# Performance work log

Measured on AMD Instinct MI355X. Metric: run time of the kernel, lower is better.

The kernel has to match this reference:

```python
import jax, jax.numpy as jnp
import numpy as np

B, N, G, P, L = 2, 6, 4, 8, 4
CIN, COUT = 256, 128
CIMG = COUT // G  # 32 per-group image channels
CAMC = 64
GX, GY, GZ = 64, 64, 4
Q = 8192
RES = (0.6, 0.6, 0.4)
PR = (-19.2, -19.2, -1.0)
IMG_W, IMG_H = 704.0, 256.0
FEAT_HW = [(32, 88), (16, 44), (8, 22), (4, 11)]


def setup_inputs():
    key = jax.random.key(0)
    ks = jax.random.split(key, 20)
    inp = {}
    for l, (H, W) in enumerate(FEAT_HW):
        inp[f"feat{l}"] = jax.random.normal(ks[l], (B, N, G * CIMG, H, W), jnp.float32)
    inp["pts_bev"] = jax.random.normal(ks[4], (B, CIN, GY, GX), jnp.float32)
    inp["lidar2img"] = jax.random.normal(ks[5], (B, N, 4, 4), jnp.float32)
    inp["query_mask"] = jnp.ones((B, Q), jnp.float32)
    inp["vox_x"] = jax.random.randint(ks[6], (B, Q), 0, GX, jnp.int32)
    inp["vox_y"] = jax.random.randint(ks[7], (B, Q), 0, GY, jnp.int32)
    inp["vox_z"] = jax.random.randint(ks[8], (B, Q), 0, GZ, jnp.int32)
    inp["w_offset"] = 0.02 * jax.random.normal(ks[9], (CIN, G * P * 3), jnp.float32)
    inp["b_offset"] = jax.random.uniform(ks[10], (G * P * 3,), jnp.float32, -0.5, 0.5)
    inp["w_scale"] = 0.02 * jax.random.normal(ks[11], (CIN, G * P * L), jnp.float32)
    inp["b_scale"] = jnp.zeros((G * P * L,), jnp.float32)
    inp["w_agg"] = 0.02 * jax.random.normal(ks[12], (P * COUT, COUT), jnp.float32)
    inp["b_agg"] = jnp.zeros((COUT,), jnp.float32)
    inp["conv1_w"] = 0.02 * jax.random.normal(ks[13], (CAMC * GZ, COUT * GZ, 3, 3), jnp.float32)
    inp["conv2_w"] = 0.02 * jax.random.normal(ks[14], (512, CAMC * GZ, 3, 3), jnp.float32)
    inp["conv3_w"] = 0.02 * jax.random.normal(ks[15], (512, 512, 3, 3), jnp.float32)
    inp["conv4_w"] = 0.02 * jax.random.normal(ks[16], (COUT, 512, 3, 3), jnp.float32)
    for i, c in zip(range(1, 5), (CAMC * GZ, 512, 512, COUT)):
        inp[f"bn{i}_g"] = jnp.ones((c,), jnp.float32)
        inp[f"bn{i}_b"] = jnp.zeros((c,), jnp.float32)
    return inp


def _bilinear(feat, bg, view, u, v):
    # feat: [BG, N, H, W, C]; u, v normalized to [0,1]; zero padding, align_corners=False
    H, W = feat.shape[2], feat.shape[3]
    px = u * W - 0.5
    py = v * H - 0.5
    x0f = jnp.floor(px)
    y0f = jnp.floor(py)
    wx = px - x0f
    wy = py - y0f
    x0 = x0f.astype(jnp.int32)
    y0 = y0f.astype(jnp.int32)

    def g(xi, yi):
        ok = ((xi >= 0) & (xi < W) & (yi >= 0) & (yi < H)).astype(feat.dtype)
        val = feat[bg, view, jnp.clip(yi, 0, H - 1), jnp.clip(xi, 0, W - 1)]
        return val * ok[..., None]

    return (g(x0, y0) * ((1 - wx) * (1 - wy))[..., None]
            + g(x0 + 1, y0) * (wx * (1 - wy))[..., None]
            + g(x0, y0 + 1) * ((1 - wx) * wy)[..., None]
            + g(x0 + 1, y0 + 1) * (wx * wy)[..., None])


def _conv_bn_relu(x, w, g, b):
    y = jax.lax.conv_general_dilated(x, w, (1, 1), 'SAME',
                                     dimension_numbers=('NCHW', 'OIHW', 'NCHW'))
    # eval-mode BatchNorm with running_mean=0, running_var=1
    y = y * (g / np.float32(np.sqrt(1.0 + 1e-5)))[None, :, None, None] + b[None, :, None, None]
    return jax.nn.relu(y)


def reference(feat0, feat1, feat2, feat3, pts_bev, lidar2img, query_mask,
              w_offset, b_offset, w_scale, b_scale, w_agg, b_agg,
              conv1_w, bn1_g, bn1_b, conv2_w, bn2_g, bn2_b,
              conv3_w, bn3_g, bn3_b, conv4_w, bn4_g, bn4_b,
              vox_x, vox_y, vox_z):
    GP = G * P
    bidx = jnp.arange(B)[:, None]
    # sparse voxel gather of BEV point features (pts_feat[i, y, x])
    pts_f = pts_bev.transpose(0, 2, 3, 1)[bidx, vox_y, vox_x]  # [B,Q,CIN]
    off = (pts_f @ w_offset + b_offset).reshape(B, Q, GP, 3)
    sw = jax.nn.softmax((pts_f @ w_scale + b_scale).reshape(B, Q, GP, L), axis=-1)
    # frustum voxel-center coords
    coord = jnp.stack([(vox_x + 0.5) * RES[0] + PR[0],
                       (vox_y + 0.5) * RES[1] + PR[1],
                       (vox_z + 0.5) * RES[2] + PR[2]], axis=-1).astype(jnp.float32)
    # make_sample_points: xy scaled by res[0], z by res[2]
    delta = off * jnp.array([RES[0], RES[0], RES[2]], jnp.float32)
    sxyz = coord[:, :, None, :] + delta  # [B,Q,GP,3]
    sp4 = jnp.concatenate([sxyz, jnp.ones_like(sxyz[..., :1])], axis=-1)
    cam = jnp.einsum('bnij,bqpj->bnqpi', lidar2img, sp4)  # [B,N,Q,GP,4]
    homo = jnp.maximum(cam[..., 2:3], 1e-5)
    uv = cam[..., 0:2] / homo / jnp.array([IMG_W, IMG_H], jnp.float32)
    valid = ((cam[..., 2] > 1e-5) & (uv[..., 0] > 0.0) & (uv[..., 0] < 1.0)
             & (uv[..., 1] > 0.0) & (uv[..., 1] < 1.0)).astype(jnp.float32)
    valid = valid.transpose(0, 2, 3, 1)  # [B,Q,GP,N]
    i_view = jnp.argmax(valid, axis=-1)  # [B,Q,GP]
    uv_q = uv.transpose(0, 2, 3, 1, 4)  # [B,Q,GP,N,2]
    idx = jnp.broadcast_to(i_view[..., None, None], (B, Q, GP, 1, 2))
    uv_sel = jnp.take_along_axis(uv_q, idx, axis=3)[..., 0, :]  # [B,Q,GP,2]
    # split heads/groups -> [B*G, Q, P, *]
    uv_bg = uv_sel.reshape(B, Q, G, P, 2).transpose(0, 2, 1, 3, 4).reshape(B * G, Q, P, 2)
    view_bg = i_view.reshape(B, Q, G, P).transpose(0, 2, 1, 3).reshape(B * G, Q, P)
    sw_bg = sw.reshape(B, Q, G, P, L).transpose(0, 2, 1, 3, 4).reshape(B * G, Q, P, L)
    bg = jnp.arange(B * G)[:, None, None]
    # msmv_sampling: multi-level multi-view bilinear sampling + softmax level weights
    out = jnp.zeros((B * G, Q, P, CIMG), jnp.float32)
    for l, f in enumerate((feat0, feat1, feat2, feat3)):
        H, W = f.shape[3], f.shape[4]
        fv = f.reshape(B, N, G, CIMG, H, W).transpose(0, 2, 1, 4, 5, 3).reshape(B * G, N, H, W, CIMG)
        out = out + sw_bg[..., l:l + 1] * _bilinear(fv, bg, view_bg, uv_bg[..., 0], uv_bg[..., 1])
    # [B,G,Q,P,C] -> [B,Q,P,G,C] -> flatten (matches final.permute(0,2,4,1,3).flatten(2))
    final = out.reshape(B, G, Q, P, CIMG).transpose(0, 2, 3, 1, 4).reshape(B, Q, P * G * CIMG)
    agg = final @ w_agg + b_agg  # [B,Q,COUT]
    # scatter back into dense BEV grid
    ffeat = jnp.zeros((B, GZ, GY, GX, COUT), jnp.float32)
    ffeat = ffeat.at[bidx, vox_z, vox_y, vox_x].add(agg * query_mask[..., None])
    x = ffeat.transpose(0, 4, 1, 2, 3).reshape(B, COUT * GZ, GY, GX)
    x = _conv_bn_relu(x, conv1_w, bn1_g, bn1_b)
    x = _conv_bn_relu(x, conv2_w, bn2_g, bn2_b)
    x = _conv_bn_relu(x, conv3_w, bn3_g, bn3_b)
    return _conv_bn_relu(x, conv4_w, bn4_g, bn4_b)
```

## Files before the change

kernel.cpp:

```cpp
#include <hip/hip_runtime.h>
#include <hip/hip_fp16.h>
#include <math.h>

#define NB    2
#define NQ    8192
#define NCIN  256
#define NG    4
#define NP    8
#define NGP   32
#define NCIMG 32
#define NCOUT 128
#define NVIEW 6
#define GXD   64
#define GYD   64
#define GZD   4

typedef float f32x4 __attribute__((ext_vector_type(4)));
typedef short s16x8 __attribute__((ext_vector_type(8)));
typedef unsigned short u16;
typedef unsigned int   u32;

__device__ __forceinline__ u16 bf16_rne(float f) {
    u32 u = __float_as_uint(f);
    u32 r = (u + 0x7FFFu + ((u >> 16) & 1u)) >> 16;
    return (u16)r;
}
__device__ __forceinline__ float bf16_f(u16 h) {
    return __uint_as_float(((u32)h) << 16);
}

__global__ void transpose_feat(const float* __restrict__ src, float* __restrict__ dst,
                               int H, int W)
{
    const int total = NB * NG * NVIEW * H * W * 32;
    for (int i = blockIdx.x * blockDim.x + threadIdx.x; i < total;
         i += gridDim.x * blockDim.x) {
        int c = i & 31;
        int r = i >> 5;
        int x = r % W;  r /= W;
        int y = r % H;  r /= H;
        int n = r % NVIEW; r /= NVIEW;
        int g = r & 3;  r >>= 2;
        int b = r;
        dst[i] = src[(((size_t)(b * NVIEW + n) * 128 + g * 32 + c) * H + y) * W + x];
    }
}

__global__ __launch_bounds__(256) void transpose_pts(const float* __restrict__ src,
                                                     float* __restrict__ dst)
{
    __shared__ float tile[64][65];
    const int tid = blockIdx.x;
    const int b = tid >> 8, rest = tid & 255;
    const int p0 = (rest >> 2) << 6, c0 = (rest & 3) << 6;
    const int t = threadIdx.x;
    for (int i = t; i < 4096; i += 256) {
        const int c = i >> 6, p = i & 63;
        tile[c][p] = src[((size_t)(b * 256 + c0 + c) << 12) + p0 + p];
    }
    __syncthreads();
    for (int i = t; i < 4096; i += 256) {
        const int p = i >> 6, c = i & 63;
        dst[((size_t)(b * 4096) + p0 + p) * 256 + c0 + c] = tile[c][p];
    }
}

__global__ void pack_wT(const float* __restrict__ w_off, const float* __restrict__ w_sc,
                        float* __restrict__ wT)
{
    int i = blockIdx.x * 256 + threadIdx.x;
    if (i >= 224 * 256) return;
    int col = i >> 8, k = i & 255;
    wT[i] = (col < 96) ? w_off[k * 96 + col] : w_sc[k * 128 + (col - 96)];
}

__global__ void pack_wagT(const float* __restrict__ w_agg, u16* __restrict__ dst)
{
    int i = blockIdx.x * 256 + threadIdx.x;
    if (i >= 128 * 1024) return;
    int co = i >> 10, k = i & 1023;
    dst[i] = bf16_rne(w_agg[k * 128 + co]);
}

__global__ void pack_conv_w(const float* __restrict__ src, u16* __restrict__ hi,
                            u16* __restrict__ lo, int CI, int CO)
{
    const int N = CO * CI * 9;
    for (int i = blockIdx.x * blockDim.x + threadIdx.x; i < N;
         i += gridDim.x * blockDim.x) {
        int tap = i % 9;
        int r = i / 9;
        int ci = r % CI;
        int co = r / CI;
        float v = src[i];
        u16 h = bf16_rne(v);
        size_t d = ((size_t)tap * CO + co) * CI + ci;
        hi[d] = h;
        lo[d] = bf16_rne(v - bf16_f(h));
    }
}

__global__ void split_x0(const float* __restrict__ x, u16* __restrict__ h,
                         u16* __restrict__ lo)
{
    const int N = NB * 4096 * 512;
    for (int i = blockIdx.x * blockDim.x + threadIdx.x; i < N;
         i += gridDim.x * blockDim.x) {
        float v = x[i];
        u16 hh = bf16_rne(v);
        h[i] = hh;
        lo[i] = bf16_rne(v - bf16_f(hh));
    }
}

__global__ __launch_bounds__(256) void fused_query8(
    const float* __restrict__ pts_cl, const float* __restrict__ l2i,
    const float* __restrict__ qmask,
    const float* __restrict__ wT, const float* __restrict__ b_off,
    const float* __restrict__ b_sc,
    const u16* __restrict__ wagT, const float* __restrict__ b_agg,
    const int* __restrict__ vxp, const int* __restrict__ vyp, const int* __restrict__ vzp,
    const float* __restrict__ fT,
    float* __restrict__ xout_cl)
{
    const int q0 = blockIdx.x << 3;
    const int b  = q0 >> 13;
    const int t  = threadIdx.x;

    __shared__ float s_pts[8][256];
    __shared__ float s_off[8][96];
    __shared__ float s_sw[8][128];
    __shared__ float s_l2i[96];
    __shared__ u32   s_toff[256][16];
    __shared__ u16   s_twgt[256][16];
    __shared__ __align__(16) u16 s_fh[8][1024];
    __shared__ __align__(16) u16 s_fl[8][1024];
    __shared__ int   s_vx[8], s_vy[8], s_vz[8];
    __shared__ float s_qm[8];

    if (t < 8) {
        s_vx[t] = vxp[q0 + t]; s_vy[t] = vyp[q0 + t]; s_vz[t] = vzp[q0 + t];
        s_qm[t] = qmask[q0 + t];
    }
    if (t < 96) s_l2i[t] = l2i[b * 96 + t];
    __syncthreads();

    #pragma unroll
    for (int q = 0; q < 8; ++q)
        s_pts[q][t] = pts_cl[((size_t)(b * 4096) + s_vy[q] * 64 + s_vx[q]) * 256 + t];
    __syncthreads();

    if (t < 224) {
        const float* __restrict__ wrow = wT + t * 256;
        const float bias = (t < 96) ? b_off[t] : b_sc[t - 96];
        float a0 = bias, a1 = bias, a2 = bias, a3 = bias;
        float a4 = bias, a5 = bias, a6 = bias, a7 = bias;
        #pragma unroll 4
        for (int k = 0; k < 256; ++k) {
            const float wk = wrow[k];
            a0 = fmaf(s_pts[0][k], wk, a0); a1 = fmaf(s_pts[1][k], wk, a1);
            a2 = fmaf(s_pts[2][k], wk, a2); a3 = fmaf(s_pts[3][k], wk, a3);
            a4 = fmaf(s_pts[4][k], wk, a4); a5 = fmaf(s_pts[5][k], wk, a5);
            a6 = fmaf(s_pts[6][k], wk, a6); a7 = fmaf(s_pts[7][k], wk, a7);
        }
        if (t < 96) {
            s_off[0][t] = a0; s_off[1][t] = a1; s_off[2][t] = a2; s_off[3][t] = a3;
            s_off[4][t] = a4; s_off[5][t] = a5; s_off[6][t] = a6; s_off[7][t] = a7;
        } else {
            const int c = t - 96;
            s_sw[0][c] = a0; s_sw[1][c] = a1; s_sw[2][c] = a2; s_sw[3][c] = a3;
            s_sw[4][c] = a4; s_sw[5][c] = a5; s_sw[6][c] = a6; s_sw[7][c] = a7;
        }
    }
    __syncthreads();

    {
        const int q = t >> 5, gp = t & 31;
        float a0 = s_sw[q][gp * 4 + 0], a1 = s_sw[q][gp * 4 + 1];
        float a2 = s_sw[q][gp * 4 + 2], a3 = s_sw[q][gp * 4 + 3];
        float m  = fmaxf(fmaxf(a0, a1), fmaxf(a2, a3));
        float e0 = expf(a0 - m), e1 = expf(a1 - m), e2 = expf(a2 - m), e3 = expf(a3 - m);
        float inv = 1.f / (e0 + e1 + e2 + e3);
        const float sw0 = e0 * inv, sw1 = e1 * inv, sw2 = e2 * inv, sw3 = e3 * inv;

        float cx = ((float)s_vx[q] + 0.5f) * 0.6f - 19.2f;
        float cy = ((float)s_vy[q] + 0.5f) * 0.6f - 19.2f;
        float cz = ((float)s_vz[q] + 0.5f) * 0.4f - 1.0f;
        float sx = cx + s_off[q][gp * 3 + 0] * 0.6f;
        float sy = cy + s_off[q][gp * 3 + 1] * 0.6f;
        float sz = cz + s_off[q][gp * 3 + 2] * 0.4f;

        int best = 0; float bu = 0.f, bv = 0.f; bool found = false;
        #pragma unroll
        for (int n = 0; n < NVIEW; ++n) {
            const float* M = &s_l2i[n * 16];
            float px = M[0] * sx + M[1] * sy + M[2]  * sz + M[3];
            float py = M[4] * sx + M[5] * sy + M[6]  * sz + M[7];
            float pz = M[8] * sx + M[9] * sy + M[10] * sz + M[11];
            float homo = fmaxf(pz, 1e-5f);
            float u = px / homo / 704.0f;
            float v = py / homo / 256.0f;
            bool val = (pz > 1e-5f) && (u > 0.f) && (u < 1.f) && (v > 0.f) && (v < 1.f);
            if (n == 0) { bu = u; bv = v; }
            if (val && !found) { found = true; best = n; bu = u; bv = v; }
        }

        const int g = gp >> 3;
        const u32 bgv = (u32)((b * 4 + g) * 6 + best);
        auto tapgen = [&](int lidx, int W, int H, u32 lbase, float swl) {
            float px = fminf(fmaxf(bu * (float)W - 0.5f, -1.0e8f), 1.0e8f);
            float py = fminf(fmaxf(bv * (float)H - 0.5f, -1.0e8f), 1.0e8f);
            float x0f = floorf(px), y0f = floorf(py);
            float wx = px - x0f, wy = py - y0f;
            int x0 = (int)x0f, y0 = (int)y0f;
            const u32 base = lbase + bgv * (u32)(H * W * 32);
            #pragma unroll
            for (int ti = 0; ti < 4; ++ti) {
                int xi = x0 + (ti & 1), yi = y0 + (ti >> 1);
                float bw = ((ti & 1) ? wx : 1.f - wx) * ((ti >> 1) ? wy : 1.f - wy);
                bool ok = ((unsigned)xi < (unsigned)W) && ((unsigned)yi < (unsigned)H);
                u32 off = ok ? (base + ((u32)(yi * W + xi) << 5)) : 0u;
                float wgt = ok ? swl * bw : 0.f;
                s_toff[t][lidx * 4 + ti] = off;
                s_twgt[t][lidx * 4 + ti] = __half_as_ushort(__float2half(wgt));
            }
        };
        tapgen(0, 88, 32, 0u,       sw0);
        tapgen(1, 44, 16, 4325376u, sw1);
        tapgen(2, 22,  8, 5406720u, sw2);
        tapgen(3, 11,  4, 5677056u, sw3);
    }
    __syncthreads();

    for (int i = t; i < 8192; i += 256) {
        const int pair = i >> 5, c = i & 31;
        float acc = 0.f;
        #pragma unroll
        for (int tp = 0; tp < 16; ++tp) {
            const u32 off = s_toff[pair][tp];
            const float wgt = __half2float(__ushort_as_half(s_twgt[pair][tp]));
            acc = fmaf(wgt, fT[off + c], acc);
        }
        const int gp = pair & 31, q = pair >> 5;
        const int g = gp >> 3, p = gp & 7;
        const int k = ((p << 2) + g) * 32 + c;
        const u16 h  = bf16_rne(acc);
        const u16 lo = bf16_rne(acc - bf16_f(h));
        const int kk = (((k >> 3) ^ q) << 3) | (k & 7);
        s_fh[q][kk] = h;
        s_fl[q][kk] = lo;
    }
    __syncthreads();

    {
        const int wv = t >> 6, l = t & 63;
        const int l15 = l & 15, kg = l >> 4;
        f32x4 acc0 = {0.f, 0.f, 0.f, 0.f}, acc1 = {0.f, 0.f, 0.f, 0.f};
        const u16* __restrict__ B0 = wagT + (((wv * 2) * 16 + l15) << 10);
        const u16* __restrict__ B1 = wagT + (((wv * 2 + 1) * 16 + l15) << 10);
        const bool realA = (l15 < 8);
        for (int ks = 0; ks < 32; ++ks) {
            s16x8 Ah = {0, 0, 0, 0, 0, 0, 0, 0};
            s16x8 Al = {0, 0, 0, 0, 0, 0, 0, 0};
            if (realA) {
                const int kk = ((((ks << 2) + kg) ^ l15) << 3);
                Ah = *reinterpret_cast<const s16x8*>(&s_fh[l15][kk]);
                Al = *reinterpret_cast<const s16x8*>(&s_fl[l15][kk]);
            }
            const int ko = (ks << 5) + (kg << 3);
            const s16x8 Bh0 = *reinterpret_cast<const s16x8*>(B0 + ko);
            const s16x8 Bh1 = *reinterpret_cast<const s16x8*>(B1 + ko);
            acc0 = __builtin_amdgcn_mfma_f32_16x16x32_bf16(Ah, Bh0, acc0, 0, 0, 0);
            acc0 = __builtin_amdgcn_mfma_f32_16x16x32_bf16(Al, Bh0, acc0, 0, 0, 0);
            acc1 = __builtin_amdgcn_mfma_f32_16x16x32_bf16(Ah, Bh1, acc1, 0, 0, 0);
            acc1 = __builtin_amdgcn_mfma_f32_16x16x32_bf16(Al, Bh1, acc1, 0, 0, 0);
        }
        if (l < 32) {
            #pragma unroll
            for (int reg = 0; reg < 4; ++reg) {
                const int q = kg * 4 + reg;
                const size_t pbase =
                    ((size_t)(b * 4096) + s_vy[q] * 64 + s_vx[q]) * 512 + s_vz[q];
                const float qm = s_qm[q];
                {
                    const int co = (wv * 2) * 16 + l15;
                    atomicAdd(&xout_cl[pbase + co * 4], (acc0[reg] + b_agg[co]) * qm);
                }
                {
                    const int co = (wv * 2 + 1) * 16 + l15;
                    atomicAdd(&xout_cl[pbase + co * 4], (acc1[reg] + b_agg[co]) * qm);
                }
            }
        }
    }
}

template<int ROWS, int NSUB, bool LAST>
__global__ __launch_bounds__(64 * ROWS * NSUB) void conv3x3_mfma2(
    const u16* __restrict__ xinh, const u16* __restrict__ xinl,
    const u16* __restrict__ whi, const u16* __restrict__ wlo,
    const float* __restrict__ gam, const float* __restrict__ bet,
    u16* __restrict__ youth, u16* __restrict__ youtl,
    float* __restrict__ ynchw, int CI, int CO)
{
    constexpr int STRIPS = 64 / ROWS;
    constexpr int NTHR = 64 * ROWS * NSUB;
    constexpr int SR = ROWS + 2;
    const int b = blockIdx.x / STRIPS, s = blockIdx.x % STRIPS;
    const int y0 = s * ROWS;
    const int co0 = blockIdx.y * (NSUB * 32);
    const int t = threadIdx.x;
    const int wid = t >> 6, l = t & 63;
    const int l15 = l & 15, kg = l >> 4;
    const int r = wid / NSUB, ns = wid % NSUB;

    __shared__ __align__(16) u16 sh[SR * 66 * 32];
    __shared__ __align__(16) u16 sl[SR * 66 * 32];

    const int coA = co0 + ns * 32 + l15;
    const int coB = coA + 16;

    f32x4 acc[4][2];
    #pragma unroll
    for (int m = 0; m < 4; ++m) {
        acc[m][0] = (f32x4){0.f, 0.f, 0.f, 0.f};
        acc[m][1] = (f32x4){0.f, 0.f, 0.f, 0.f};
    }

    for (int cc = 0; cc < CI; cc += 32) {
        __syncthreads();
        for (int i = t; i < SR * 66 * 4; i += NTHR) {
            const int cb = i & 3, r2 = i >> 2;
            const int xx = r2 % 66, rr = r2 / 66;
            const int yi = y0 - 1 + rr, xi = xx - 1;
            uint4 H = {0, 0, 0, 0}, L = {0, 0, 0, 0};
            if ((unsigned)yi < 64u && (unsigned)xi < 64u) {
                const size_t src = ((size_t)(b * 4096 + yi * 64 + xi)) * CI + cc + cb * 8;
                H = *reinterpret_cast<const uint4*>(xinh + src);
                L = *reinterpret_cast<const uint4*>(xinl + src);
            }
            const int off = (rr * 66 + xx) * 32 + ((cb ^ ((xx ^ (xx >> 2)) & 3)) << 3);
            *reinterpret_cast<uint4*>(&sh[off]) = H;
            *reinterpret_cast<uint4*>(&sl[off]) = L;
        }
        __syncthreads();

        #pragma unroll
        for (int tap = 0; tap < 9; ++tap) {
            const int ky = tap / 3, kx = tap % 3;
            const size_t woA = ((size_t)tap * CO + coA) * CI + cc + kg * 8;
            const size_t woB = ((size_t)tap * CO + coB) * CI + cc + kg * 8;
            const s16x8 BhA = *reinterpret_cast<const s16x8*>(whi + woA);
            const s16x8 BlA = *reinterpret_cast<const s16x8*>(wlo + woA);
            const s16x8 BhB = *reinterpret_cast<const s16x8*>(whi + woB);
            const s16x8 BlB = *reinterpret_cast<const s16x8*>(wlo + woB);
            #pragma unroll
            for (int m = 0; m < 4; ++m) {
                const int xx = m * 16 + l15 + kx;
                const int off = ((r + ky) * 66 + xx) * 32
                              + ((kg ^ ((xx ^ (xx >> 2)) & 3)) << 3);
                const s16x8 Ah = *reinterpret_cast<const s16x8*>(&sh[off]);
                const s16x8 Al = *reinterpret_cast<const s16x8*>(&sl[off]);
                acc[m][0] = __builtin_amdgcn_mfma_f32_16x16x32_bf16(Ah, BhA, acc[m][0], 0, 0, 0);
                acc[m][0] = __builtin_amdgcn_mfma_f32_16x16x32_bf16(Ah, BlA, acc[m][0], 0, 0, 0);
                acc[m][0] = __builtin_amdgcn_mfma_f32_16x16x32_bf16(Al, BhA, acc[m][0], 0, 0, 0);
                acc[m][1] = __builtin_amdgcn_mfma_f32_16x16x32_bf16(Ah, BhB, acc[m][1], 0, 0, 0);
                acc[m][1] = __builtin_amdgcn_mfma_f32_16x16x32_bf16(Ah, BlB, acc[m][1], 0, 0, 0);
                acc[m][1] = __builtin_amdgcn_mfma_f32_16x16x32_bf16(Al, BhB, acc[m][1], 0, 0, 0);
            }
        }
    }

    const float inv = 0.99999500003749978f;
    const int row = y0 + r;
    #pragma unroll
    for (int j = 0; j < 2; ++j) {
        const int co = j ? coB : coA;
        const float gsc = gam[co] * inv;
        const float bta = bet[co];
        #pragma unroll
        for (int m = 0; m < 4; ++m) {
            #pragma unroll
            for (int reg = 0; reg < 4; ++reg) {
                const int x = m * 16 + kg * 4 + reg;
                const float val = fmaxf(fmaf(acc[m][j][reg], gsc, bta), 0.f);
                if (LAST) {
                    ynchw[(((size_t)(b * CO + co)) << 12) + row * 64 + x] = val;
                } else {
                    const size_t idx = ((size_t)(b * 4096 + row * 64 + x)) * CO + co;
                    const u16 h = bf16_rne(val);
                    youth[idx] = h;
                    youtl[idx] = bf16_rne(val - bf16_f(h));
                }
            }
        }
    }
}

extern "C" void kernel_launch(void* const* d_in, const int* in_sizes, int n_in,
                              void* d_out, int out_size, void* d_ws, size_t ws_size,
                              hipStream_t stream)
{
    const float* feat0    = (const float*)d_in[0];
    const float* feat1    = (const float*)d_in[1];
    const float* feat2    = (const float*)d_in[2];
    const float* feat3    = (const float*)d_in[3];
    const float* pts_bev  = (const float*)d_in[4];
    const float* l2i      = (const float*)d_in[5];
    const float* qmask    = (const float*)d_in[6];
    const int*   vox_x    = (const int*)d_in[7];
    const int*   vox_y    = (const int*)d_in[8];
    const int*   vox_z    = (const int*)d_in[9];
    const float* w_off    = (const float*)d_in[10];
    const float* b_off    = (const float*)d_in[11];
    const float* w_sc     = (const float*)d_in[12];
    const float* b_sc     = (const float*)d_in[13];
    const float* w_agg    = (const float*)d_in[14];
    const float* b_agg    = (const float*)d_in[15];
    const float* conv1_w  = (const float*)d_in[16];
    const float* conv2_w  = (const float*)d_in[17];
    const float* conv3_w  = (const float*)d_in[18];
    const float* conv4_w  = (const float*)d_in[19];
    const float* bn1_g    = (const float*)d_in[20];
    const float* bn1_b    = (const float*)d_in[21];
    const float* bn2_g    = (const float*)d_in[22];
    const float* bn2_b    = (const float*)d_in[23];
    const float* bn3_g    = (const float*)d_in[24];
    const float* bn3_b    = (const float*)d_in[25];
    const float* bn4_g    = (const float*)d_in[26];
    const float* bn4_b    = (const float*)d_in[27];

    char* wsb = (char*)d_ws;
    float* fT0 = (float*)wsb;
    float* fT1 = fT0 + 4325376;
    float* fT2 = fT1 + 1081344;
    float* fT3 = fT2 + 270336;
    u16* wpk = (u16*)wsb;
    u16* wh1 = wpk;             u16* wl1 = wpk + 1179648;
    u16* wh2 = wpk + 2359296;   u16* wl2 = wpk + 3538944;
    u16* wh3 = wpk + 4718592;   u16* wl3 = wpk + 7077888;
    u16* wh4 = wpk + 9437184;   u16* wl4 = wpk + 10027008;
    float* x0f   = (float*)(wsb + 22978560);
    u16*   x2h   = (u16*)(wsb + 22978560);   u16* x2l = x2h + 4194304;
    float* ptsCL = (float*)(wsb + 39755776);
    u16*   x0h   = (u16*)(wsb + 39755776);
    u16*   x0l   = (u16*)(wsb + 48144384);
    u16*   x3h   = x0h;                      u16* x3l = x0l;
    u16*   x1h   = (u16*)(wsb + 56532992);   u16* x1l = x1h + 2097152;
    u16*   wagT  = (u16*)(wsb + 48144384);
    float* wTp   = (float*)(wsb + 48406528);

    pack_wT<<<224, 256, 0, stream>>>(w_off, w_sc, wTp);
    pack_wagT<<<512, 256, 0, stream>>>(w_agg, wagT);
    transpose_pts<<<512, 256, 0, stream>>>(pts_bev, ptsCL);

    transpose_feat<<<1024, 256, 0, stream>>>(feat0, fT0, 32, 88);
    transpose_feat<<< 512, 256, 0, stream>>>(feat1, fT1, 16, 44);
    transpose_feat<<< 128, 256, 0, stream>>>(feat2, fT2,  8, 22);
    transpose_feat<<<  64, 256, 0, stream>>>(feat3, fT3,  4, 11);

    hipMemsetAsync(x0f, 0, (size_t)4194304 * sizeof(float), stream);

    fused_query8<<<NB * NQ / 8, 256, 0, stream>>>(
        ptsCL, l2i, qmask, wTp, b_off, b_sc, wagT, b_agg,
        vox_x, vox_y, vox_z, fT0, x0f);

    pack_conv_w<<<1024, 256, 0, stream>>>(conv1_w, wh1, wl1, 512, 256);
    pack_conv_w<<<1024, 256, 0, stream>>>(conv2_w, wh2, wl2, 256, 512);
    pack_conv_w<<<2048, 256, 0, stream>>>(conv3_w, wh3, wl3, 512, 512);
    pack_conv_w<<< 512, 256, 0, stream>>>(conv4_w, wh4, wl4, 512, 128);

    split_x0<<<4096, 256, 0, stream>>>(x0f, x0h, x0l);

    conv3x3_mfma2<2, 2, false><<<dim3(64, 4), 256, 0, stream>>>(
        x0h, x0l, wh1, wl1, bn1_g, bn1_b, x1h, x1l, nullptr, 512, 256);
    conv3x3_mfma2<2, 2, false><<<dim3(64, 8), 256, 0, stream>>>(
        x1h, x1l, wh2, wl2, bn2_g, bn2_b, x2h, x2l, nullptr, 256, 512);
    conv3x3_mfma2<2, 2, false><<<dim3(64, 8), 256, 0, stream>>>(
        x2h, x2l, wh3, wl3, bn3_g, bn3_b, x3h, x3l, nullptr, 512, 512);
    conv3x3_mfma2<1, 2, true><<<dim3(128, 2), 128, 0, stream>>>(
        x3h, x3l, wh4, wl4, bn4_g, bn4_b, nullptr, nullptr, (float*)d_out, 512, 128);
}
```

Measured before the change: 891.5 us.

## Switch conv chain to single fp16 MFMA and use MFMA for offset projection

The four 3x3 convs move from split-bf16 (three MFMAs per product, hi/lo activations and weights) to single-pass fp16 MFMA, with a new double-buffered LDS tile of one output row and 64 output channels per block. The offset/scale projection in the query kernel becomes a split-bf16 MFMA GEMM instead of scalar FMAs. The sampling loop now uses float4 channel loads, and LDS buffers are unioned to cut shared memory use. This removes much of the MFMA and memory traffic in the convs, but fp16 precision and range may loosen accuracy against the fp32 reference.

After: 1.170 ms. 31.2% more time.

```diff
diff --git a/kernel.cpp b/kernel.cpp
--- a/kernel.cpp
+++ b/kernel.cpp
@@ -17,6 +17,7 @@
 
 typedef float f32x4 __attribute__((ext_vector_type(4)));
 typedef short s16x8 __attribute__((ext_vector_type(8)));
+typedef _Float16 f16x8 __attribute__((ext_vector_type(8)));
 typedef unsigned short u16;
 typedef unsigned int   u32;
 
@@ -27,6 +28,9 @@
 }
 __device__ __forceinline__ float bf16_f(u16 h) {
     return __uint_as_float(((u32)h) << 16);
+}
+__device__ __forceinline__ u16 f16_u(float f) {
+    return __half_as_ushort(__float2half(f));
 }
 
 __global__ void transpose_feat(const float* __restrict__ src, float* __restrict__ dst,
@@ -65,13 +69,18 @@
     }
 }
 
-__global__ void pack_wT(const float* __restrict__ w_off, const float* __restrict__ w_sc,
-                        float* __restrict__ wT)
+__global__ void pack_wT_split(const float* __restrict__ w_off,
+                              const float* __restrict__ w_sc,
+                              u16* __restrict__ wTh, u16* __restrict__ wTl)
 {
     int i = blockIdx.x * 256 + threadIdx.x;
-    if (i >= 224 * 256) return;
+    if (i >= 256 * 256) return;
     int col = i >> 8, k = i & 255;
-    wT[i] = (col < 96) ? w_off[k * 96 + col] : w_sc[k * 128 + (col - 96)];
+    float v = (col < 96) ? w_off[k * 96 + col]
+            : (col < 224 ? w_sc[k * 128 + (col - 96)] : 0.f);
+    u16 h = bf16_rne(v);
+    wTh[col * 256 + k] = h;
+    wTl[col * 256 + k] = bf16_rne(v - bf16_f(h));
 }
 
 __global__ void pack_wagT(const float* __restrict__ w_agg, u16* __restrict__ dst)
@@ -82,8 +91,8 @@
     dst[i] = bf16_rne(w_agg[k * 128 + co]);
 }
 
-__global__ void pack_conv_w(const float* __restrict__ src, u16* __restrict__ hi,
-                            u16* __restrict__ lo, int CI, int CO)
+__global__ void pack_conv_w_f16(const float* __restrict__ src, u16* __restrict__ dst,
+                                int CI, int CO)
 {
     const int N = CO * CI * 9;
     for (int i = blockIdx.x * blockDim.x + threadIdx.x; i < N;
@@ -92,32 +101,27 @@
         int r = i / 9;
         int ci = r % CI;
         int co = r / CI;
-        float v = src[i];
-        u16 h = bf16_rne(v);
-        size_t d = ((size_t)tap * CO + co) * CI + ci;
-        hi[d] = h;
-        lo[d] = bf16_rne(v - bf16_f(h));
-    }
-}
-
-__global__ void split_x0(const float* __restrict__ x, u16* __restrict__ h,
-                         u16* __restrict__ lo)
-{
-    const int N = NB * 4096 * 512;
-    for (int i = blockIdx.x * blockDim.x + threadIdx.x; i < N;
+        dst[((size_t)tap * CO + co) * CI + ci] = f16_u(src[i]);
+    }
+}
+
+__global__ void cvt_x0(const float* __restrict__ x, u16* __restrict__ y)
+{
+    const int N4 = NB * 4096 * 512 / 4;
+    for (int i = blockIdx.x * blockDim.x + threadIdx.x; i < N4;
          i += gridDim.x * blockDim.x) {
-        float v = x[i];
-        u16 hh = bf16_rne(v);
-        h[i] = hh;
-        lo[i] = bf16_rne(v - bf16_f(hh));
+        float4 v = reinterpret_cast<const float4*>(x)[i];
+        u32 lo = (u32)f16_u(v.x) | ((u32)f16_u(v.y) << 16);
+        u32 hi = (u32)f16_u(v.z) | ((u32)f16_u(v.w) << 16);
+        reinterpret_cast<uint2*>(y)[i] = make_uint2(lo, hi);
     }
 }
 
 __global__ __launch_bounds__(256) void fused_query8(
     const float* __restrict__ pts_cl, const float* __restrict__ l2i,
     const float* __restrict__ qmask,
-    const float* __restrict__ wT, const float* __restrict__ b_off,
-    const float* __restrict__ b_sc,
+    const u16* __restrict__ wTh, const u16* __restrict__ wTl,
+    const float* __restrict__ b_off, const float* __restrict__ b_sc,
     const u16* __restrict__ wagT, const float* __restrict__ b_agg,
     const int* __restrict__ vxp, const int* __restrict__ vyp, const int* __restrict__ vzp,
     const float* __restrict__ fT,
@@ -127,16 +131,19 @@
     const int b  = q0 >> 13;
     const int t  = threadIdx.x;
 
-    __shared__ float s_pts[8][256];
+    __shared__ __align__(16) u16 s_ph[8][256];
+    __shared__ __align__(16) u16 s_pl[8][256];
     __shared__ float s_off[8][96];
     __shared__ float s_sw[8][128];
     __shared__ float s_l2i[96];
-    __shared__ u32   s_toff[256][16];
-    __shared__ u16   s_twgt[256][16];
-    __shared__ __align__(16) u16 s_fh[8][1024];
-    __shared__ __align__(16) u16 s_fl[8][1024];
+    __shared__ __align__(16) char s_un[32768];
     __shared__ int   s_vx[8], s_vy[8], s_vz[8];
     __shared__ float s_qm[8];
+
+    u32  (*s_toff)[16]  = reinterpret_cast<u32 (*)[16]>(s_un);
+    u16  (*s_twgt)[16]  = reinterpret_cast<u16 (*)[16]>(s_un + 16384);
+    u16  (*s_fh)[1024]  = reinterpret_cast<u16 (*)[1024]>(s_un);
+    u16  (*s_fl)[1024]  = reinterpret_cast<u16 (*)[1024]>(s_un + 16384);
 
     if (t < 8) {
         s_vx[t] = vxp[q0 + t]; s_vy[t] = vyp[q0 + t]; s_vz[t] = vzp[q0 + t];
@@ -145,31 +152,59 @@
     if (t < 96) s_l2i[t] = l2i[b * 96 + t];
     __syncthreads();
 
-    #pragma unroll
-    for (int q = 0; q < 8; ++q)
-        s_pts[q][t] = pts_cl[((size_t)(b * 4096) + s_vy[q] * 64 + s_vx[q]) * 256 + t];
-    __syncthreads();
-
-    if (t < 224) {
-        const float* __restrict__ wrow = wT + t * 256;
-        const float bias = (t < 96) ? b_off[t] : b_sc[t - 96];
-        float a0 = bias, a1 = bias, a2 = bias, a3 = bias;
-        float a4 = bias, a5 = bias, a6 = bias, a7 = bias;
-        #pragma unroll 4
-        for (int k = 0; k < 256; ++k) {
-            const float wk = wrow[k];
-            a0 = fmaf(s_pts[0][k], wk, a0); a1 = fmaf(s_pts[1][k], wk, a1);
-            a2 = fmaf(s_pts[2][k], wk, a2); a3 = fmaf(s_pts[3][k], wk, a3);
-            a4 = fmaf(s_pts[4][k], wk, a4); a5 = fmaf(s_pts[5][k], wk, a5);
-            a6 = fmaf(s_pts[6][k], wk, a6); a7 = fmaf(s_pts[7][k], wk, a7);
-        }
-        if (t < 96) {
-            s_off[0][t] = a0; s_off[1][t] = a1; s_off[2][t] = a2; s_off[3][t] = a3;
-            s_off[4][t] = a4; s_off[5][t] = a5; s_off[6][t] = a6; s_off[7][t] = a7;
-        } else {
-            const int c = t - 96;
-            s_sw[0][c] = a0; s_sw[1][c] = a1; s_sw[2][c] = a2; s_sw[3][c] = a3;
-            s_sw[4][c] = a4; s_sw[5][c] = a5; s_sw[6][c] = a6; s_sw[7][c] = a7;
+    {
+        const int q = t >> 5, c8 = t & 31;
+        const float4* p = reinterpret_cast<const float4*>(
+            pts_cl + ((size_t)(b * 4096) + s_vy[q] * 64 + s_vx[q]) * 256 + c8 * 8);
+        float4 v0 = p[0], v1 = p[1];
+        float v[8] = {v0.x, v0.y, v0.z, v0.w, v1.x, v1.y, v1.z, v1.w};
+        union { u16 u[8]; uint4 q4; } H, L;
+        #pragma unroll
+        for (int j = 0; j < 8; ++j) {
+            u16 h = bf16_rne(v[j]);
+            H.u[j] = h;
+            L.u[j] = bf16_rne(v[j] - bf16_f(h));
+        }
+        const int kb = c8 ^ q;
+        *reinterpret_cast<uint4*>(&s_ph[q][kb * 8]) = H.q4;
+        *reinterpret_cast<uint4*>(&s_pl[q][kb * 8]) = L.q4;
+    }
+    __syncthreads();
+
+    {
+        const int wv = t >> 6, l = t & 63;
+        const int l15 = l & 15, kg = l >> 4;
+        const int qa = l15 & 7;
+        f32x4 acc[4];
+        #pragma unroll
+        for (int nf = 0; nf < 4; ++nf) acc[nf] = (f32x4){0.f, 0.f, 0.f, 0.f};
+        #pragma unroll
+        for (int ks = 0; ks < 8; ++ks) {
+            const int kb = (ks * 4 + kg) ^ qa;
+            const s16x8 Ah = *reinterpret_cast<const s16x8*>(&s_ph[qa][kb * 8]);
+            const s16x8 Al = *reinterpret_cast<const s16x8*>(&s_pl[qa][kb * 8]);
+            #pragma unroll
+            for (int nf = 0; nf < 4; ++nf) {
+                const int col = wv * 64 + nf * 16 + l15;
+                const size_t wo = (size_t)col * 256 + ks * 32 + kg * 8;
+                const s16x8 Bh = *reinterpret_cast<const s16x8*>(wTh + wo);
+                const s16x8 Bl = *reinterpret_cast<const s16x8*>(wTl + wo);
+                acc[nf] = __builtin_amdgcn_mfma_f32_16x16x32_bf16(Ah, Bh, acc[nf], 0, 0, 0);
+                acc[nf] = __builtin_amdgcn_mfma_f32_16x16x32_bf16(Ah, Bl, acc[nf], 0, 0, 0);
+                acc[nf] = __builtin_amdgcn_mfma_f32_16x16x32_bf16(Al, Bh, acc[nf], 0, 0, 0);
+            }
+        }
+        if (kg < 2) {
+            #pragma unroll
+            for (int nf = 0; nf < 4; ++nf) {
+                const int col = wv * 64 + nf * 16 + l15;
+                #pragma unroll
+                for (int reg = 0; reg < 4; ++reg) {
+                    const int q = kg * 4 + reg;
+                    if (col < 96)        s_off[q][col]      = acc[nf][reg] + b_off[col];
+                    else if (col < 224)  s_sw[q][col - 96]  = acc[nf][reg] + b_sc[col - 96];
+                }
+            }
         }
     }
     __syncthreads();
@@ -222,7 +257,7 @@
                 u32 off = ok ? (base + ((u32)(yi * W + xi) << 5)) : 0u;
                 float wgt = ok ? swl * bw : 0.f;
                 s_toff[t][lidx * 4 + ti] = off;
-                s_twgt[t][lidx * 4 + ti] = __half_as_ushort(__float2half(wgt));
+                s_twgt[t][lidx * 4 + ti] = f16_u(wgt);
             }
         };
         tapgen(0, 88, 32, 0u,       sw0);
@@ -232,41 +267,55 @@
     }
     __syncthreads();
 
-    for (int i = t; i < 8192; i += 256) {
-        const int pair = i >> 5, c = i & 31;
-        float acc = 0.f;
+    f32x4 sacc[8];
+    #pragma unroll
+    for (int j = 0; j < 8; ++j) {
+        const int pair = (j * 256 + t) >> 3, c4 = t & 7;
+        const u32* toff = s_toff[pair];
+        const u16* twgt = s_twgt[pair];
+        f32x4 a = (f32x4){0.f, 0.f, 0.f, 0.f};
         #pragma unroll
         for (int tp = 0; tp < 16; ++tp) {
-            const u32 off = s_toff[pair][tp];
-            const float wgt = __half2float(__ushort_as_half(s_twgt[pair][tp]));
-            acc = fmaf(wgt, fT[off + c], acc);
-        }
-        const int gp = pair & 31, q = pair >> 5;
+            const float w = __half2float(__ushort_as_half(twgt[tp]));
+            const float4 f = *reinterpret_cast<const float4*>(fT + toff[tp] + c4 * 4);
+            a[0] = fmaf(w, f.x, a[0]); a[1] = fmaf(w, f.y, a[1]);
+            a[2] = fmaf(w, f.z, a[2]); a[3] = fmaf(w, f.w, a[3]);
+        }
+        sacc[j] = a;
+    }
+    __syncthreads();
+
+    #pragma unroll
+    for (int j = 0; j < 8; ++j) {
+        const int pair = (j * 256 + t) >> 3, c4 = t & 7;
+        const int q = pair >> 5, gp = pair & 31;
         const int g = gp >> 3, p = gp & 7;
-        const int k = ((p << 2) + g) * 32 + c;
-        const u16 h  = bf16_rne(acc);
-        const u16 lo = bf16_rne(acc - bf16_f(h));
-        const int kk = (((k >> 3) ^ q) << 3) | (k & 7);
-        s_fh[q][kk] = h;
-        s_fl[q][kk] = lo;
+        const int kb = ((p << 2) + g) * 4 + (c4 >> 1);
+        const int off = ((kb ^ q) << 3) + (c4 & 1) * 4;
+        u16 h[4], lo[4];
+        #pragma unroll
+        for (int e = 0; e < 4; ++e) {
+            h[e]  = bf16_rne(sacc[j][e]);
+            lo[e] = bf16_rne(sacc[j][e] - bf16_f(h[e]));
+        }
+        *reinterpret_cast<uint2*>(&s_fh[q][off]) =
+            make_uint2((u32)h[0] | ((u32)h[1] << 16), (u32)h[2] | ((u32)h[3] << 16));
+        *reinterpret_cast<uint2*>(&s_fl[q][off]) =
+            make_uint2((u32)lo[0] | ((u32)lo[1] << 16), (u32)lo[2] | ((u32)lo[3] << 16));
     }
     __syncthreads();
 
     {
         const int wv = t >> 6, l = t & 63;
         const int l15 = l & 15, kg = l >> 4;
+        const int qa = l15 & 7;
         f32x4 acc0 = {0.f, 0.f, 0.f, 0.f}, acc1 = {0.f, 0.f, 0.f, 0.f};
         const u16* __restrict__ B0 = wagT + (((wv * 2) * 16 + l15) << 10);
         const u16* __restrict__ B1 = wagT + (((wv * 2 + 1) * 16 + l15) << 10);
-        const bool realA = (l15 < 8);
         for (int ks = 0; ks < 32; ++ks) {
-            s16x8 Ah = {0, 0, 0, 0, 0, 0, 0, 0};
-            s16x8 Al = {0, 0, 0, 0, 0, 0, 0, 0};
-            if (realA) {
-                const int kk = ((((ks << 2) + kg) ^ l15) << 3);
-                Ah = *reinterpret_cast<const s16x8*>(&s_fh[l15][kk]);
-                Al = *reinterpret_cast<const s16x8*>(&s_fl[l15][kk]);
-            }
+            const int kk = ((((ks << 2) + kg) ^ qa) << 3);
+            const s16x8 Ah = *reinterpret_cast<const s16x8*>(&s_fh[qa][kk]);
+            const s16x8 Al = *reinterpret_cast<const s16x8*>(&s_fl[qa][kk]);
             const int ko = (ks << 5) + (kg << 3);
             const s16x8 Bh0 = *reinterpret_cast<const s16x8*>(B0 + ko);
             const s16x8 Bh1 = *reinterpret_cast<const s16x8*>(B1 + ko);
@@ -295,103 +344,100 @@
     }
 }
 
-template<int ROWS, int NSUB, bool LAST>
-__global__ __launch_bounds__(64 * ROWS * NSUB) void conv3x3_mfma2(
-    const u16* __restrict__ xinh, const u16* __restrict__ xinl,
-    const u16* __restrict__ whi, const u16* __restrict__ wlo,
+template<bool LAST>
+__global__ __launch_bounds__(256) void conv3x3_f16(
+    const u16* __restrict__ xin,
+    const u16* __restrict__ wf,
     const float* __restrict__ gam, const float* __restrict__ bet,
-    u16* __restrict__ youth, u16* __restrict__ youtl,
-    float* __restrict__ ynchw, int CI, int CO)
-{
-    constexpr int STRIPS = 64 / ROWS;
-    constexpr int NTHR = 64 * ROWS * NSUB;
-    constexpr int SR = ROWS + 2;
-    const int b = blockIdx.x / STRIPS, s = blockIdx.x % STRIPS;
-    const int y0 = s * ROWS;
-    const int co0 = blockIdx.y * (NSUB * 32);
+    u16* __restrict__ yf16, float* __restrict__ ynchw, int CI, int CO)
+{
+    const int b  = blockIdx.x >> 6;
+    const int y0 = blockIdx.x & 63;
+    const int co0 = blockIdx.y << 6;
     const int t = threadIdx.x;
-    const int wid = t >> 6, l = t & 63;
+    const int wv = t >> 6, l = t & 63;
     const int l15 = l & 15, kg = l >> 4;
-    const int r = wid / NSUB, ns = wid % NSUB;
-
-    __shared__ __align__(16) u16 sh[SR * 66 * 32];
-    __shared__ __align__(16) u16 sl[SR * 66 * 32];
-
-    const int coA = co0 + ns * 32 + l15;
-    const int coB = coA + 16;
-
-    f32x4 acc[4][2];
-    #pragma unroll
-    for (int m = 0; m < 4; ++m) {
-        acc[m][0] = (f32x4){0.f, 0.f, 0.f, 0.f};
-        acc[m][1] = (f32x4){0.f, 0.f, 0.f, 0.f};
-    }
-
+
+    __shared__ __align__(16) u16 lds[2][3 * 66 * 32];
+
+    const int cnt = (t < 24) ? 4 : 3;
+    size_t soff[4]; int loff[4]; bool sval[4];
+    #pragma unroll
+    for (int k = 0; k < 4; ++k) {
+        const int i = t + k * 256;
+        const int cb = i & 3, xr = i >> 2;
+        const int x = xr % 66, r = xr / 66;
+        const int yi = y0 - 1 + r, xi = x - 1;
+        sval[k] = ((unsigned)yi < 64u) && ((unsigned)xi < 64u) && (i < 792);
+        soff[k] = ((size_t)(b * 4096 + yi * 64 + xi)) * CI + cb * 8;
+        loff[k] = (r * 66 + x) * 32 + cb * 8;
+    }
+
+    f32x4 acc[4];
+    #pragma unroll
+    for (int nf = 0; nf < 4; ++nf) acc[nf] = (f32x4){0.f, 0.f, 0.f, 0.f};
+
+    const uint4 Z = make_uint4(0u, 0u, 0u, 0u);
+    uint4 st[4];
+    #pragma unroll
+    for (int k = 0; k < 4; ++k)
+        if (k < cnt) st[k] = sval[k] ? *reinterpret_cast<const uint4*>(xin + soff[k]) : Z;
+    #pragma unroll
+    for (int k = 0; k < 4; ++k)
+        if (k < cnt && (t + k * 256) < 792)
+            *reinterpret_cast<uint4*>(&lds[0][loff[k]]) = st[k];
+    __syncthreads();
+
+    int cur = 0;
     for (int cc = 0; cc < CI; cc += 32) {
+        const bool more = (cc + 32 < CI);
+        if (more) {
+            #pragma unroll
+            for (int k = 0; k < 4; ++k)
+                if (k < cnt)
+                    st[k] = sval[k]
+                          ? *reinterpret_cast<const uint4*>(xin + soff[k] + cc + 32) : Z;
+        }
+        #pragma unroll
+        for (int ky = 0; ky < 3; ++ky) {
+            #pragma unroll
+            for (int kx = 0; kx < 3; ++kx) {
+                const f16x8 A = *reinterpret_cast<const f16x8*>(
+                    &lds[cur][(ky * 66 + wv * 16 + l15 + kx) * 32 + kg * 8]);
+                const int tap = ky * 3 + kx;
+                #pragma unroll
+                for (int nf = 0; nf < 4; ++nf) {
+                    const int co = co0 + nf * 16 + l15;
+                    const f16x8 B = *reinterpret_cast<const f16x8*>(
+                        wf + ((size_t)tap * CO + co) * CI + cc + kg * 8);
+                    acc[nf] = __builtin_amdgcn_mfma_f32_16x16x32_f16(A, B, acc[nf], 0, 0, 0);
+                }
+            }
+        }
+        if (more) {
+            #pragma unroll
+            for (int k = 0; k < 4; ++k)
+                if (k < cnt && (t + k * 256) < 792)
+                    *reinterpret_cast<uint4*>(&lds[cur ^ 1][loff[k]]) = st[k];
+        }
         __syncthreads();
-        for (int i = t; i < SR * 66 * 4; i += NTHR) {
-            const int cb = i & 3, r2 = i >> 2;
-            const int xx = r2 % 66, rr = r2 / 66;
-            const int yi = y0 - 1 + rr, xi = xx - 1;
-            uint4 H = {0, 0, 0, 0}, L = {0, 0, 0, 0};
-            if ((unsigned)yi < 64u && (unsigned)xi < 64u) {
-                const size_t src = ((size_t)(b * 4096 + yi * 64 + xi)) * CI + cc + cb * 8;
-                H = *reinterpret_cast<const uint4*>(xinh + src);
-                L = *reinterpret_cast<const uint4*>(xinl + src);
-            }
-            const int off = (rr * 66 + xx) * 32 + ((cb ^ ((xx ^ (xx >> 2)) & 3)) << 3);
-            *reinterpret_cast<uint4*>(&sh[off]) = H;
-            *reinterpret_cast<uint4*>(&sl[off]) = L;
-        }
-        __syncthreads();
-
-        #pragma unroll
-        for (int tap = 0; tap < 9; ++tap) {
-            const int ky = tap / 3, kx = tap % 3;
-            const size_t woA = ((size_t)tap * CO + coA) * CI + cc + kg * 8;
-            const size_t woB = ((size_t)tap * CO + coB) * CI + cc + kg * 8;
-            const s16x8 BhA = *reinterpret_cast<const s16x8*>(whi + woA);
-            const s16x8 BlA = *reinterpret_cast<const s16x8*>(wlo + woA);
-            const s16x8 BhB = *reinterpret_cast<const s16x8*>(whi + woB);
-            const s16x8 BlB = *reinterpret_cast<const s16x8*>(wlo + woB);
-            #pragma unroll
-            for (int m = 0; m < 4; ++m) {
-                const int xx = m * 16 + l15 + kx;
-                const int off = ((r + ky) * 66 + xx) * 32
-                              + ((kg ^ ((xx ^ (xx >> 2)) & 3)) << 3);
-                const s16x8 Ah = *reinterpret_cast<const s16x8*>(&sh[off]);
-                const s16x8 Al = *reinterpret_cast<const s16x8*>(&sl[off]);
-                acc[m][0] = __builtin_amdgcn_mfma_f32_16x16x32_bf16(Ah, BhA, acc[m][0], 0, 0, 0);
-                acc[m][0] = __builtin_amdgcn_mfma_f32_16x16x32_bf16(Ah, BlA, acc[m][0], 0, 0, 0);
-                acc[m][0] = __builtin_amdgcn_mfma_f32_16x16x32_bf16(Al, BhA, acc[m][0], 0, 0, 0);
-                acc[m][1] = __builtin_amdgcn_mfma_f32_16x16x32_bf16(Ah, BhB, acc[m][1], 0, 0, 0);
-                acc[m][1] = __builtin_amdgcn_mfma_f32_16x16x32_bf16(Ah, BlB, acc[m][1], 0, 0, 0);
-                acc[m][1] = __builtin_amdgcn_mfma_f32_16x16x32_bf16(Al, BhB, acc[m][1], 0, 0, 0);
-            }
-        }
+        cur ^= 1;
     }
 
     const float inv = 0.99999500003749978f;
-    const int row = y0 + r;
-    #pragma unroll
-    for (int j = 0; j < 2; ++j) {
-        const int co = j ? coB : coA;
+    #pragma unroll
+    for (int nf = 0; nf < 4; ++nf) {
+        const int co = co0 + nf * 16 + l15;
         const float gsc = gam[co] * inv;
         const float bta = bet[co];
         #pragma unroll
-        for (int m = 0; m < 4; ++m) {
-            #pragma unroll
-            for (int reg = 0; reg < 4; ++reg) {
-                const int x = m * 16 + kg * 4 + reg;
-                const float val = fmaxf(fmaf(acc[m][j][reg], gsc, bta), 0.f);
-                if (LAST) {
-                    ynchw[(((size_t)(b * CO + co)) << 12) + row * 64 + x] = val;
-                } else {
-                    const size_t idx = ((size_t)(b * 4096 + row * 64 + x)) * CO + co;
-                    const u16 h = bf16_rne(val);
-                    youth[idx] = h;
-                    youtl[idx] = bf16_rne(val - bf16_f(h));
-                }
+        for (int reg = 0; reg < 4; ++reg) {
+            const int px = wv * 16 + kg * 4 + reg;
+            const float val = fmaxf(fmaf(acc[nf][reg], gsc, bta), 0.f);
+            if (LAST) {
+                ynchw[(((size_t)(b * CO + co)) << 12) + y0 * 64 + px] = val;
+            } else {
+                yf16[((size_t)(b * 4096 + y0 * 64 + px)) * CO + co] = f16_u(val);
             }
         }
     }
@@ -436,21 +482,21 @@
     float* fT2 = fT1 + 1081344;
     float* fT3 = fT2 + 270336;
     u16* wpk = (u16*)wsb;
-    u16* wh1 = wpk;             u16* wl1 = wpk + 1179648;
-    u16* wh2 = wpk + 2359296;   u16* wl2 = wpk + 3538944;
-    u16* wh3 = wpk + 4718592;   u16* wl3 = wpk + 7077888;
-    u16* wh4 = wpk + 9437184;   u16* wl4 = wpk + 10027008;
+    u16* w1f = wpk;
+    u16* w2f = wpk + 1179648;
+    u16* w3f = wpk + 2359296;
+    u16* w4f = wpk + 4718592;
     float* x0f   = (float*)(wsb + 22978560);
-    u16*   x2h   = (u16*)(wsb + 22978560);   u16* x2l = x2h + 4194304;
+    u16*   x2f   = (u16*)(wsb + 22978560);
     float* ptsCL = (float*)(wsb + 39755776);
     u16*   x0h   = (u16*)(wsb + 39755776);
-    u16*   x0l   = (u16*)(wsb + 48144384);
-    u16*   x3h   = x0h;                      u16* x3l = x0l;
-    u16*   x1h   = (u16*)(wsb + 56532992);   u16* x1l = x1h + 2097152;
-    u16*   wagT  = (u16*)(wsb + 48144384);
-    float* wTp   = (float*)(wsb + 48406528);
-
-    pack_wT<<<224, 256, 0, stream>>>(w_off, w_sc, wTp);
+    u16*   x3f   = x0h;
+    u16*   x1f   = (u16*)(wsb + 48144384);
+    u16*   wTh   = (u16*)(wsb + 52338688);
+    u16*   wTl   = (u16*)(wsb + 52469760);
+    u16*   wagT  = (u16*)(wsb + 52600832);
+
+    pack_wT_split<<<256, 256, 0, stream>>>(w_off, w_sc, wTh, wTl);
     pack_wagT<<<512, 256, 0, stream>>>(w_agg, wagT);
     transpose_pts<<<512, 256, 0, stream>>>(pts_bev, ptsCL);
 
@@ -462,22 +508,22 @@
     hipMemsetAsync(x0f, 0, (size_t)4194304 * sizeof(float), stream);
 
     fused_query8<<<NB * NQ / 8, 256, 0, stream>>>(
-        ptsCL, l2i, qmask, wTp, b_off, b_sc, wagT, b_agg,
+        ptsCL, l2i, qmask, wTh, wTl, b_off, b_sc, wagT, b_agg,
         vox_x, vox_y, vox_z, fT0, x0f);
 
-    pack_conv_w<<<1024, 256, 0, stream>>>(conv1_w, wh1, wl1, 512, 256);
-    pack_conv_w<<<1024, 256, 0, stream>>>(conv2_w, wh2, wl2, 256, 512);
-    pack_conv_w<<<2048, 256, 0, stream>>>(conv3_w, wh3, wl3, 512, 512);
-    pack_conv_w<<< 512, 256, 0, stream>>>(conv4_w, wh4, wl4, 512, 128);
-
-    split_x0<<<4096, 256, 0, stream>>>(x0f, x0h, x0l);
-
-    conv3x3_mfma2<2, 2, false><<<dim3(64, 4), 256, 0, stream>>>(
-        x0h, x0l, wh1, wl1, bn1_g, bn1_b, x1h, x1l, nullptr, 512, 256);
-    conv3x3_mfma2<2, 2, false><<<dim3(64, 8), 256, 0, stream>>>(
-        x1h, x1l, wh2, wl2, bn2_g, bn2_b, x2h, x2l, nullptr, 256, 512);
-    conv3x3_mfma2<2, 2, false><<<dim3(64, 8), 256, 0, stream>>>(
-        x2h, x2l, wh3, wl3, bn3_g, bn3_b, x3h, x3l, nullptr, 512, 512);
-    conv3x3_mfma2<1, 2, true><<<dim3(128, 2), 128, 0, stream>>>(
-        x3h, x3l, wh4, wl4, bn4_g, bn4_b, nullptr, nullptr, (float*)d_out, 512, 128);
-}
+    pack_conv_w_f16<<<1024, 256, 0, stream>>>(conv1_w, w1f, 512, 256);
+    pack_conv_w_f16<<<1024, 256, 0, stream>>>(conv2_w, w2f, 256, 512);
+    pack_conv_w_f16<<<2048, 256, 0, stream>>>(conv3_w, w3f, 512, 512);
+    pack_conv_w_f16<<< 512, 256, 0, stream>>>(conv4_w, w4f, 512, 128);
+
+    cvt_x0<<<1024, 256, 0, stream>>>(x0f, x0h);
+
+    conv3x3_f16<false><<<dim3(NB * 64, 4), 256, 0, stream>>>(
+        x0h, w1f, bn1_g, bn1_b, x1f, nullptr, 512, 256);
+    conv3x3_f16<false><<<dim3(NB * 64, 8), 256, 0, stream>>>(
+        x1f, w2f, bn2_g, bn2_b, x2f, nullptr, 256, 512);
+    conv3x3_f16<false><<<dim3(NB * 64, 8), 256, 0, stream>>>(
+        x2f, w3f, bn3_g, bn3_b, x3f, nullptr, 512, 512);
+    conv3x3_f16<true><<<dim3(NB * 64, 2), 256, 0, stream>>>(
+        x3f, w4f, bn4_g, bn4_b, nullptr, (float*)d_out, 512, 128);
+}
```
